# Performance work log

Hardware: AMD Instinct MI355X
Metric: run time of the kernel (lower is better)

Reference implementation:

```python
import jax, jax.numpy as jnp
import numpy as np

B, S, D, H = 4, 2048, 768, 12
DK = D // H


def setup_inputs() -> dict:
    key = jax.random.key(0)
    ks = jax.random.split(key, 13)
    s = 1.0 / np.sqrt(D)
    inp = {
        "q": jax.random.normal(ks[0], (B, S, D), jnp.float32),
        "k": jax.random.normal(ks[1], (B, S, D), jnp.float32),
        "v": jax.random.normal(ks[2], (B, S, D), jnp.float32),
        "mask": jax.random.randint(ks[3], (B, S), 0, 2, jnp.int32),
        "Wq": jax.random.normal(ks[4], (D, D), jnp.float32) * s,
        "bq": jnp.zeros((D,), jnp.float32),
        "Wk": jax.random.normal(ks[5], (D, D), jnp.float32) * s,
        "bk": jnp.zeros((D,), jnp.float32),
        "Wv": jax.random.normal(ks[6], (D, D), jnp.float32) * s,
        "bv": jnp.zeros((D,), jnp.float32),
        "Wo": jax.random.normal(ks[7], (D, D), jnp.float32) * s,
        "bo": jnp.zeros((D,), jnp.float32),
    }
    return inp


def reference(q, k, v, mask, Wq, bq, Wk, bk, Wv, bv, Wo, bo):
    b, s, d = q.shape
    # projections (torch Linear: x @ W.T + b), split into heads: [b, h, s, dk]
    Q = (q @ Wq.T + bq).reshape(b, s, H, DK).transpose(0, 2, 1, 3)
    K = (k @ Wk.T + bk).reshape(b, s, H, DK).transpose(0, 2, 1, 3)
    V = (v @ Wv.T + bv).reshape(b, s, H, DK).transpose(0, 2, 1, 3)
    scores = jnp.einsum("bhqd,bhkd->bhqk", Q, K) / jnp.sqrt(jnp.float32(DK))
    # mask [b,s] -> [b,1,s,1]: masks whole query rows (faithful to source)
    scores = jnp.where(mask[:, None, :, None] == 0, jnp.float32(-1e9), scores)
    attn = jax.nn.softmax(scores, axis=-1)  # dropout is identity at inference
    out = jnp.einsum("bhqk,bhkd->bhqd", attn, V)
    concat = out.transpose(0, 2, 1, 3).reshape(b, s, d)
    return concat @ Wo.T + bo
```

## Files before the change

### kernel.cpp

```cpp
#include <hip/hip_runtime.h>

typedef _Float16 f16;
typedef f16 f16x4 __attribute__((ext_vector_type(4)));
typedef f16 f16x8 __attribute__((ext_vector_type(8)));
typedef float f32x4 __attribute__((ext_vector_type(4)));

#define B_ 4
#define S_ 2048
#define D_ 768
#define H_ 12
#define DK_ 64

__device__ __forceinline__ void dma16(const f16* g, f16* l) {
    __builtin_amdgcn_global_load_lds(
        (__attribute__((address_space(1))) void*)(uintptr_t)g,
        (__attribute__((address_space(3))) void*)l, 16, 0, 0);
}

struct Cvt7 { const float* s[7]; f16* d[7]; int n[7]; };

__global__ __launch_bounds__(256) void cvt7_kernel(Cvt7 a)
{
    const int z = blockIdx.y;
    int i = (blockIdx.x * 256 + threadIdx.x) * 8;
    if (i >= a.n[z]) return;
    const float* __restrict__ s = a.s[z];
    float4 x = *(const float4*)(s + i);
    float4 y = *(const float4*)(s + i + 4);
    f16x8 h = {(f16)x.x, (f16)x.y, (f16)x.z, (f16)x.w,
               (f16)y.x, (f16)y.y, (f16)y.z, (f16)y.w};
    *(f16x8*)(a.d[z] + i) = h;
}

struct GemmArgs { const f16* A; const f16* W; const float* bias; float scale; void* C; int mode; };
struct GemmArgs3 { GemmArgs g[3]; };

__global__ __launch_bounds__(256, 4) void gemm_k(GemmArgs3 args)
{
    const int z = blockIdx.z;
    const f16* __restrict__ A = args.g[z].A;
    const f16* __restrict__ W = args.g[z].W;
    const float* __restrict__ bias = args.g[z].bias;
    const float scale = args.g[z].scale;
    const int mode = args.g[z].mode;

    __shared__ __align__(16) f16 As[128 * 64];
    __shared__ __align__(16) f16 Bs[128 * 64];

    const int tid = threadIdx.x, lane = tid & 63, w = tid >> 6;
    const int l15 = lane & 15, lg = lane >> 4;
    const int wm = (w >> 1) * 64, wn = (w & 1) * 64;
    const int m0 = blockIdx.y * 128, n0 = blockIdx.x * 128;

    const int lrow8 = lane >> 3;
    const int lchk8 = (lane & 7) ^ lrow8;
    const f16* gA = A + (size_t)(m0 + w * 32 + lrow8) * D_ + lchk8 * 8;
    const f16* gB = W + (size_t)(n0 + w * 32 + lrow8) * D_ + lchk8 * 8;

    f32x4 acc[4][4] = {};

    for (int kt = 0; kt < D_; kt += 64) {
        __syncthreads();
#pragma unroll
        for (int c = 0; c < 4; ++c) {
            dma16(gA + (size_t)(c * 8) * D_ + kt, &As[(w * 4 + c) * 512]);
            dma16(gB + (size_t)(c * 8) * D_ + kt, &Bs[(w * 4 + c) * 512]);
        }
        __syncthreads();
#pragma unroll
        for (int kk = 0; kk < 2; ++kk) {
            const int chk = ((kk * 4 + lg) ^ (l15 & 7)) * 8;
            f16x8 af[4], bf[4];
#pragma unroll
            for (int i = 0; i < 4; ++i)
                af[i] = *(const f16x8*)&As[(wm + i * 16 + l15) * 64 + chk];
#pragma unroll
            for (int j = 0; j < 4; ++j)
                bf[j] = *(const f16x8*)&Bs[(wn + j * 16 + l15) * 64 + chk];
#pragma unroll
            for (int i = 0; i < 4; ++i)
#pragma unroll
                for (int j = 0; j < 4; ++j)
                    acc[i][j] = __builtin_amdgcn_mfma_f32_16x16x32_f16(
                        af[i], bf[j], acc[i][j], 0, 0, 0);
        }
    }

    if (mode == 1) {
#pragma unroll
        for (int j = 0; j < 4; ++j) {
            int col = n0 + wn + j * 16 + l15;
            float bb = bias[col];
#pragma unroll
            for (int i = 0; i < 4; ++i) {
                int row = m0 + wm + i * 16 + lg * 4;
                int bI = row >> 11, sl = row & (S_ - 1);
                f16x4 o = {(f16)(acc[i][j][0] + bb), (f16)(acc[i][j][1] + bb),
                           (f16)(acc[i][j][2] + bb), (f16)(acc[i][j][3] + bb)};
                *(f16x4*)&((f16*)args.g[z].C)[((size_t)bI * D_ + col) * S_ + sl] = o;
            }
        }
    } else if (mode == 0) {
#pragma unroll
        for (int j = 0; j < 4; ++j) {
            int col = n0 + wn + j * 16 + l15;
            float bb = bias[col];
#pragma unroll
            for (int i = 0; i < 4; ++i) {
                int row = m0 + wm + i * 16 + lg * 4;
#pragma unroll
                for (int r = 0; r < 4; ++r)
                    ((f16*)args.g[z].C)[(size_t)(row + r) * D_ + col] =
                        (f16)((acc[i][j][r] + bb) * scale);
            }
        }
    } else {
#pragma unroll
        for (int j = 0; j < 4; ++j) {
            int col = n0 + wn + j * 16 + l15;
            float bb = bias[col];
#pragma unroll
            for (int i = 0; i < 4; ++i) {
                int row = m0 + wm + i * 16 + lg * 4;
#pragma unroll
                for (int r = 0; r < 4; ++r)
                    ((float*)args.g[z].C)[(size_t)(row + r) * D_ + col] =
                        acc[i][j][r] + bb;
            }
        }
    }
}

__global__ __launch_bounds__(256, 3) void attn_k(
    const f16* __restrict__ Qh, const f16* __restrict__ Kh,
    const f16* __restrict__ VhT, const int* __restrict__ mask,
    f16* __restrict__ O)
{
    __shared__ __align__(16) f16 Ks[128 * 64];
    __shared__ __align__(16) f16 Vt[64 * 128];
    const int tid = threadIdx.x, lane = tid & 63, w = tid >> 6;
    const int l15 = lane & 15, lg = lane >> 4;

    const int bid = blockIdx.x;
    const int g8 = bid & 7, j5 = bid >> 3;
    const int head_lin = g8 * 6 + (j5 >> 4);
    const int qt = j5 & 15;
    const int b = head_lin / H_, h = head_lin % H_;
    const int q0 = qt * 128;
    const int rowbase = b * S_;
    const int col0 = h * DK_;

    const int lrow8 = lane >> 3;
    const int lchk8 = (lane & 7) ^ lrow8;

    {
        const f16* Qbase = Qh + (size_t)(rowbase + q0 + w * 32 + lrow8) * D_ + col0 + lchk8 * 8;
#pragma unroll
        for (int c = 0; c < 4; ++c)
            dma16(Qbase + (size_t)(c * 8) * D_, &Ks[(w * 4 + c) * 512]);
    }
    __syncthreads();
    f16x8 qf[2][2];
#pragma unroll
    for (int ns = 0; ns < 2; ++ns) {
        float mf = (mask[rowbase + q0 + w * 32 + ns * 16 + l15] != 0) ? 1.0f : 0.0f;
#pragma unroll
        for (int kk = 0; kk < 2; ++kk) {
            f16x8 t = *(const f16x8*)&Ks[(w * 32 + ns * 16 + l15) * 64 +
                                         (((kk * 4 + lg) ^ (l15 & 7)) * 8)];
#pragma unroll
            for (int e = 0; e < 8; ++e) t[e] = (f16)((float)t[e] * mf);
            qf[ns][kk] = t;
        }
    }

    const f16* Kbase = Kh + (size_t)rowbase * D_ + col0;
    const f16* Vbase = VhT + ((size_t)b * D_ + col0) * S_;
    const int vrow4 = lane >> 4;
    const int vchk = lane & 15;

    float lrun[2] = {0.f, 0.f};
    f32x4 acc[4][2] = {};

    for (int t = 0; t < S_ / 128; ++t) {
        const int k0 = t * 128;
        __syncthreads();
#pragma unroll
        for (int c = 0; c < 4; ++c)
            dma16(Kbase + (size_t)(k0 + w * 32 + c * 8 + lrow8) * D_ + lchk8 * 8,
                  &Ks[(w * 4 + c) * 512]);
#pragma unroll
        for (int c = 0; c < 4; ++c) {
            int o = w * 4 + c;
            int drow = o * 4 + vrow4;
            int gchk = vchk ^ (drow & 15);
            dma16(Vbase + (size_t)drow * S_ + k0 + gchk * 8, &Vt[o * 512]);
        }
        __syncthreads();

        f32x4 sf[8][2] = {};
#pragma unroll
        for (int kk = 0; kk < 2; ++kk) {
            const int chk = ((kk * 4 + lg) ^ (l15 & 7)) * 8;
#pragma unroll
            for (int ms = 0; ms < 8; ++ms) {
                f16x8 kf = *(const f16x8*)&Ks[(ms * 16 + l15) * 64 + chk];
                sf[ms][0] = __builtin_amdgcn_mfma_f32_16x16x32_f16(
                    kf, qf[0][kk], sf[ms][0], 0, 0, 0);
                sf[ms][1] = __builtin_amdgcn_mfma_f32_16x16x32_f16(
                    kf, qf[1][kk], sf[ms][1], 0, 0, 0);
            }
        }

        f16x4 pf[8][2];
#pragma unroll
        for (int ns = 0; ns < 2; ++ns) {
            float rs = 0.f;
#pragma unroll
            for (int ms = 0; ms < 8; ++ms) {
                float p0 = __builtin_exp2f(sf[ms][ns][0]);
                float p1 = __builtin_exp2f(sf[ms][ns][1]);
                float p2 = __builtin_exp2f(sf[ms][ns][2]);
                float p3 = __builtin_exp2f(sf[ms][ns][3]);
                rs += (p0 + p1) + (p2 + p3);
                pf[ms][ns] = {(f16)p0, (f16)p1, (f16)p2, (f16)p3};
            }
            rs += __shfl_xor(rs, 16, 64);
            rs += __shfl_xor(rs, 32, 64);
            lrun[ns] += rs;
        }

#pragma unroll
        for (int c = 0; c < 8; ++c) {
            const int pchk = (((c * 2 + (lg >> 1)) ^ l15) * 8) + (lg & 1) * 4;
#pragma unroll
            for (int i = 0; i < 4; ++i) {
                f16x4 vf = *(const f16x4*)&Vt[(i * 16 + l15) * 128 + pchk];
                acc[i][0] = __builtin_amdgcn_mfma_f32_16x16x16f16(
                    vf, pf[c][0], acc[i][0], 0, 0, 0);
                acc[i][1] = __builtin_amdgcn_mfma_f32_16x16x16f16(
                    vf, pf[c][1], acc[i][1], 0, 0, 0);
            }
        }
    }

#pragma unroll
    for (int ns = 0; ns < 2; ++ns) {
        float inv = 1.0f / lrun[ns];
        size_t qrow = (size_t)(rowbase + q0 + w * 32 + ns * 16 + l15);
#pragma unroll
        for (int i = 0; i < 4; ++i) {
            f32x4 o = acc[i][ns] * inv;
            f16x4 ho = {(f16)o[0], (f16)o[1], (f16)o[2], (f16)o[3]};
            *(f16x4*)&O[qrow * D_ + col0 + i * 16 + lg * 4] = ho;
        }
    }
}

extern "C" void kernel_launch(void* const* d_in, const int* in_sizes, int n_in,
                              void* d_out, int out_size, void* d_ws, size_t ws_size,
                              hipStream_t stream)
{
    const float* q    = (const float*)d_in[0];
    const float* k    = (const float*)d_in[1];
    const float* v    = (const float*)d_in[2];
    const int*   mask = (const int*)d_in[3];
    const float* Wq   = (const float*)d_in[4];
    const float* bq   = (const float*)d_in[5];
    const float* Wk   = (const float*)d_in[6];
    const float* bk   = (const float*)d_in[7];
    const float* Wv   = (const float*)d_in[8];
    const float* bv   = (const float*)d_in[9];
    const float* Wo   = (const float*)d_in[10];
    const float* bo   = (const float*)d_in[11];

    const size_t nQKV = (size_t)B_ * S_ * D_;
    const size_t nW   = (size_t)D_ * D_;

    f16* qh  = (f16*)d_ws;
    f16* kh  = qh + nQKV;
    f16* vh  = kh + nQKV;
    f16* Wqh = vh + nQKV;
    f16* Wkh = Wqh + nW;
    f16* Wvh = Wkh + nW;
    f16* Woh = Wvh + nW;
    f16* Qp  = Woh + nW;
    f16* Kp  = Qp + nQKV;
    f16* VpT = Kp + nQKV;
    f16* Cp  = VpT + nQKV;

    Cvt7 cv = {{q, k, v, Wq, Wk, Wv, Wo},
               {qh, kh, vh, Wqh, Wkh, Wvh, Woh},
               {(int)nQKV, (int)nQKV, (int)nQKV, (int)nW, (int)nW, (int)nW, (int)nW}};
    cvt7_kernel<<<dim3((int)(nQKV / 8 / 256), 7), 256, 0, stream>>>(cv);

    GemmArgs3 g1 = {{{qh, Wqh, bq, 1.44269504f / 8.0f, (void*)Qp, 0},
                     {kh, Wkh, bk, 1.0f, (void*)Kp, 0},
                     {vh, Wvh, bv, 1.0f, (void*)VpT, 1}}};
    gemm_k<<<dim3(6, 64, 3), 256, 0, stream>>>(g1);

    attn_k<<<dim3(768), 256, 0, stream>>>(Qp, Kp, VpT, mask, Cp);

    GemmArgs3 g2 = {{{Cp, Woh, bo, 1.0f, d_out, 2},
                     {Cp, Woh, bo, 1.0f, d_out, 2},
                     {Cp, Woh, bo, 1.0f, d_out, 2}}};
    gemm_k<<<dim3(6, 64, 1), 256, 0, stream>>>(g2);
}
```

Before: 296.6 us.

## Double-buffer GEMM and attention LDS tiles and compute softmax row sums via MFMA

The projection GEMM now uses two K=32 LDS buffers and prefetches the next tile while computing on the current one, with a new 4-chunk swizzle. The attention kernel double-buffers its K/V tiles so the next tile's DMA overlaps the current QK^T, exp and PV work, and occupancy is lowered to 2 blocks per CU. Row sums come from an extra MFMA against a ones vector, replacing per-lane adds and cross-lane shuffles. The aim is to hide global load latency and cut VALU and shuffle work, at the cost of doubled LDS and lower occupancy.

```diff
diff --git a/kernel.cpp b/kernel.cpp
--- a/kernel.cpp
+++ b/kernel.cpp
@@ -44,46 +44,54 @@
     const float scale = args.g[z].scale;
     const int mode = args.g[z].mode;
 
-    __shared__ __align__(16) f16 As[128 * 64];
-    __shared__ __align__(16) f16 Bs[128 * 64];
+    __shared__ __align__(16) f16 As[2][128 * 32];
+    __shared__ __align__(16) f16 Bs[2][128 * 32];
 
     const int tid = threadIdx.x, lane = tid & 63, w = tid >> 6;
     const int l15 = lane & 15, lg = lane >> 4;
     const int wm = (w >> 1) * 64, wn = (w & 1) * 64;
     const int m0 = blockIdx.y * 128, n0 = blockIdx.x * 128;
 
-    const int lrow8 = lane >> 3;
-    const int lchk8 = (lane & 7) ^ lrow8;
-    const f16* gA = A + (size_t)(m0 + w * 32 + lrow8) * D_ + lchk8 * 8;
-    const f16* gB = W + (size_t)(n0 + w * 32 + lrow8) * D_ + lchk8 * 8;
+    const int r16 = lane >> 2;
+    const int rswS = (r16 & 3) ^ ((r16 >> 2) & 3);
+    const int gch = (lane & 3) ^ rswS;
+    const f16* gA = A + (size_t)(m0 + w * 32 + r16) * D_ + gch * 8;
+    const f16* gB = W + (size_t)(n0 + w * 32 + r16) * D_ + gch * 8;
+    const int rs15 = (l15 & 3) ^ ((l15 >> 2) & 3);
 
     f32x4 acc[4][4] = {};
-
-    for (int kt = 0; kt < D_; kt += 64) {
+    const int NIT = D_ / 32;
+
+#pragma unroll
+    for (int c = 0; c < 2; ++c) {
+        dma16(gA + (size_t)(c * 16) * D_, &As[0][(w * 2 + c) * 512]);
+        dma16(gB + (size_t)(c * 16) * D_, &Bs[0][(w * 2 + c) * 512]);
+    }
+
+    for (int t = 0; t < NIT; ++t) {
         __syncthreads();
-#pragma unroll
-        for (int c = 0; c < 4; ++c) {
-            dma16(gA + (size_t)(c * 8) * D_ + kt, &As[(w * 4 + c) * 512]);
-            dma16(gB + (size_t)(c * 8) * D_ + kt, &Bs[(w * 4 + c) * 512]);
-        }
-        __syncthreads();
-#pragma unroll
-        for (int kk = 0; kk < 2; ++kk) {
-            const int chk = ((kk * 4 + lg) ^ (l15 & 7)) * 8;
-            f16x8 af[4], bf[4];
-#pragma unroll
-            for (int i = 0; i < 4; ++i)
-                af[i] = *(const f16x8*)&As[(wm + i * 16 + l15) * 64 + chk];
+        if (t + 1 < NIT) {
+            const int kt = (t + 1) * 32, nb = (t + 1) & 1;
+#pragma unroll
+            for (int c = 0; c < 2; ++c) {
+                dma16(gA + (size_t)(c * 16) * D_ + kt, &As[nb][(w * 2 + c) * 512]);
+                dma16(gB + (size_t)(c * 16) * D_ + kt, &Bs[nb][(w * 2 + c) * 512]);
+            }
+        }
+        const int cb = t & 1;
+        f16x8 af[4], bf[4];
+#pragma unroll
+        for (int i = 0; i < 4; ++i)
+            af[i] = *(const f16x8*)&As[cb][(wm + i * 16 + l15) * 32 + ((lg ^ rs15) * 8)];
+#pragma unroll
+        for (int j = 0; j < 4; ++j)
+            bf[j] = *(const f16x8*)&Bs[cb][(wn + j * 16 + l15) * 32 + ((lg ^ rs15) * 8)];
+#pragma unroll
+        for (int i = 0; i < 4; ++i)
 #pragma unroll
             for (int j = 0; j < 4; ++j)
-                bf[j] = *(const f16x8*)&Bs[(wn + j * 16 + l15) * 64 + chk];
-#pragma unroll
-            for (int i = 0; i < 4; ++i)
-#pragma unroll
-                for (int j = 0; j < 4; ++j)
-                    acc[i][j] = __builtin_amdgcn_mfma_f32_16x16x32_f16(
-                        af[i], bf[j], acc[i][j], 0, 0, 0);
-        }
+                acc[i][j] = __builtin_amdgcn_mfma_f32_16x16x32_f16(
+                    af[i], bf[j], acc[i][j], 0, 0, 0);
     }
 
     if (mode == 1) {
@@ -131,13 +139,13 @@
     }
 }
 
-__global__ __launch_bounds__(256, 3) void attn_k(
+__global__ __launch_bounds__(256, 2) void attn_k(
     const f16* __restrict__ Qh, const f16* __restrict__ Kh,
     const f16* __restrict__ VhT, const int* __restrict__ mask,
     f16* __restrict__ O)
 {
-    __shared__ __align__(16) f16 Ks[128 * 64];
-    __shared__ __align__(16) f16 Vt[64 * 128];
+    __shared__ __align__(16) f16 Ks[2][128 * 64];
+    __shared__ __align__(16) f16 Vt[2][64 * 128];
     const int tid = threadIdx.x, lane = tid & 63, w = tid >> 6;
     const int l15 = lane & 15, lg = lane >> 4;
 
@@ -153,50 +161,65 @@
     const int lrow8 = lane >> 3;
     const int lchk8 = (lane & 7) ^ lrow8;
 
-    {
-        const f16* Qbase = Qh + (size_t)(rowbase + q0 + w * 32 + lrow8) * D_ + col0 + lchk8 * 8;
-#pragma unroll
-        for (int c = 0; c < 4; ++c)
-            dma16(Qbase + (size_t)(c * 8) * D_, &Ks[(w * 4 + c) * 512]);
-    }
-    __syncthreads();
-    f16x8 qf[2][2];
-#pragma unroll
-    for (int ns = 0; ns < 2; ++ns) {
-        float mf = (mask[rowbase + q0 + w * 32 + ns * 16 + l15] != 0) ? 1.0f : 0.0f;
-#pragma unroll
-        for (int kk = 0; kk < 2; ++kk) {
-            f16x8 t = *(const f16x8*)&Ks[(w * 32 + ns * 16 + l15) * 64 +
-                                         (((kk * 4 + lg) ^ (l15 & 7)) * 8)];
-#pragma unroll
-            for (int e = 0; e < 8; ++e) t[e] = (f16)((float)t[e] * mf);
-            qf[ns][kk] = t;
-        }
-    }
-
     const f16* Kbase = Kh + (size_t)rowbase * D_ + col0;
     const f16* Vbase = VhT + ((size_t)b * D_ + col0) * S_;
     const int vrow4 = lane >> 4;
     const int vchk = lane & 15;
 
-    float lrun[2] = {0.f, 0.f};
-    f32x4 acc[4][2] = {};
-
-    for (int t = 0; t < S_ / 128; ++t) {
-        const int k0 = t * 128;
-        __syncthreads();
+    {
+        const f16* Qb = Qh + (size_t)(rowbase + q0 + w * 32 + lrow8) * D_ + col0 + lchk8 * 8;
 #pragma unroll
         for (int c = 0; c < 4; ++c)
-            dma16(Kbase + (size_t)(k0 + w * 32 + c * 8 + lrow8) * D_ + lchk8 * 8,
-                  &Ks[(w * 4 + c) * 512]);
+            dma16(Qb + (size_t)(c * 8) * D_, &Ks[1][(w * 4 + c) * 512]);
+#pragma unroll
+        for (int c = 0; c < 4; ++c)
+            dma16(Kbase + (size_t)(w * 32 + c * 8 + lrow8) * D_ + lchk8 * 8,
+                  &Ks[0][(w * 4 + c) * 512]);
 #pragma unroll
         for (int c = 0; c < 4; ++c) {
             int o = w * 4 + c;
             int drow = o * 4 + vrow4;
-            int gchk = vchk ^ (drow & 15);
-            dma16(Vbase + (size_t)drow * S_ + k0 + gchk * 8, &Vt[o * 512]);
-        }
-        __syncthreads();
+            dma16(Vbase + (size_t)drow * S_ + (vchk ^ (drow & 15)) * 8,
+                  &Vt[0][o * 512]);
+        }
+    }
+    __syncthreads();
+
+    f16x8 qf[2][2];
+#pragma unroll
+    for (int ns = 0; ns < 2; ++ns) {
+        float mf = (mask[rowbase + q0 + w * 32 + ns * 16 + l15] != 0) ? 1.0f : 0.0f;
+#pragma unroll
+        for (int kk = 0; kk < 2; ++kk) {
+            f16x8 t = *(const f16x8*)&Ks[1][(w * 32 + ns * 16 + l15) * 64 +
+                                           (((kk * 4 + lg) ^ (l15 & 7)) * 8)];
+#pragma unroll
+            for (int e = 0; e < 8; ++e) t[e] = (f16)((float)t[e] * mf);
+            qf[ns][kk] = t;
+        }
+    }
+    __syncthreads();
+
+    const f16x4 kones = {(f16)1.f, (f16)1.f, (f16)1.f, (f16)1.f};
+    f32x4 acc[4][2] = {};
+    f32x4 acc_l[2] = {};
+
+    for (int t = 0; t < S_ / 128; ++t) {
+        if (t + 1 < S_ / 128) {
+            const int k0 = (t + 1) * 128, nb = (t + 1) & 1;
+#pragma unroll
+            for (int c = 0; c < 4; ++c)
+                dma16(Kbase + (size_t)(k0 + w * 32 + c * 8 + lrow8) * D_ + lchk8 * 8,
+                      &Ks[nb][(w * 4 + c) * 512]);
+#pragma unroll
+            for (int c = 0; c < 4; ++c) {
+                int o = w * 4 + c;
+                int drow = o * 4 + vrow4;
+                dma16(Vbase + (size_t)drow * S_ + k0 + (vchk ^ (drow & 15)) * 8,
+                      &Vt[nb][o * 512]);
+            }
+        }
+        const int cb = t & 1;
 
         f32x4 sf[8][2] = {};
 #pragma unroll
@@ -204,7 +227,7 @@
             const int chk = ((kk * 4 + lg) ^ (l15 & 7)) * 8;
 #pragma unroll
             for (int ms = 0; ms < 8; ++ms) {
-                f16x8 kf = *(const f16x8*)&Ks[(ms * 16 + l15) * 64 + chk];
+                f16x8 kf = *(const f16x8*)&Ks[cb][(ms * 16 + l15) * 64 + chk];
                 sf[ms][0] = __builtin_amdgcn_mfma_f32_16x16x32_f16(
                     kf, qf[0][kk], sf[ms][0], 0, 0, 0);
                 sf[ms][1] = __builtin_amdgcn_mfma_f32_16x16x32_f16(
@@ -214,39 +237,39 @@
 
         f16x4 pf[8][2];
 #pragma unroll
-        for (int ns = 0; ns < 2; ++ns) {
-            float rs = 0.f;
+        for (int ns = 0; ns < 2; ++ns)
 #pragma unroll
             for (int ms = 0; ms < 8; ++ms) {
                 float p0 = __builtin_exp2f(sf[ms][ns][0]);
                 float p1 = __builtin_exp2f(sf[ms][ns][1]);
                 float p2 = __builtin_exp2f(sf[ms][ns][2]);
                 float p3 = __builtin_exp2f(sf[ms][ns][3]);
-                rs += (p0 + p1) + (p2 + p3);
                 pf[ms][ns] = {(f16)p0, (f16)p1, (f16)p2, (f16)p3};
             }
-            rs += __shfl_xor(rs, 16, 64);
-            rs += __shfl_xor(rs, 32, 64);
-            lrun[ns] += rs;
-        }
 
 #pragma unroll
         for (int c = 0; c < 8; ++c) {
             const int pchk = (((c * 2 + (lg >> 1)) ^ l15) * 8) + (lg & 1) * 4;
 #pragma unroll
             for (int i = 0; i < 4; ++i) {
-                f16x4 vf = *(const f16x4*)&Vt[(i * 16 + l15) * 128 + pchk];
+                f16x4 vf = *(const f16x4*)&Vt[cb][(i * 16 + l15) * 128 + pchk];
                 acc[i][0] = __builtin_amdgcn_mfma_f32_16x16x16f16(
                     vf, pf[c][0], acc[i][0], 0, 0, 0);
                 acc[i][1] = __builtin_amdgcn_mfma_f32_16x16x16f16(
                     vf, pf[c][1], acc[i][1], 0, 0, 0);
             }
-        }
+            acc_l[0] = __builtin_amdgcn_mfma_f32_16x16x16f16(
+                kones, pf[c][0], acc_l[0], 0, 0, 0);
+            acc_l[1] = __builtin_amdgcn_mfma_f32_16x16x16f16(
+                kones, pf[c][1], acc_l[1], 0, 0, 0);
+        }
+
+        __syncthreads();
     }
 
 #pragma unroll
     for (int ns = 0; ns < 2; ++ns) {
-        float inv = 1.0f / lrun[ns];
+        float inv = 1.0f / acc_l[ns][0];
         size_t qrow = (size_t)(rowbase + q0 + w * 32 + ns * 16 + l15);
 #pragma unroll
         for (int i = 0; i < 4; ++i) {
```

New measurement: 318.5 us. 1.07x slower.

## Split attention key range across two blocks and combine partial results

Applied to the files above, without the earlier changes.

Splits each query tile's key loop into two halves handled by separate blocks (1536 blocks instead of 768). Each block writes unnormalized fp16 partial outputs and row sums, and a new combine kernel adds the halves and normalizes. Row sums are now computed with an extra MFMA against a ones vector instead of shuffles. Occupancy hint is raised to 4 and LDS addressing is precomputed. The split adds an extra kernel launch and extra global traffic for the partials, and the unnormalized partials are rounded to fp16, which could cost accuracy. Because there is no running max, correctness relies on Q being pre-scaled as before.

```diff
diff --git a/kernel.cpp b/kernel.cpp
--- a/kernel.cpp
+++ b/kernel.cpp
@@ -131,10 +131,11 @@
     }
 }
 
-__global__ __launch_bounds__(256, 3) void attn_k(
+__global__ __launch_bounds__(256, 4) void attn_k(
     const f16* __restrict__ Qh, const f16* __restrict__ Kh,
     const f16* __restrict__ VhT, const int* __restrict__ mask,
-    f16* __restrict__ O)
+    f16* __restrict__ Np0, f16* __restrict__ Np1,
+    float* __restrict__ Lp0, float* __restrict__ Lp1)
 {
     __shared__ __align__(16) f16 Ks[128 * 64];
     __shared__ __align__(16) f16 Vt[64 * 128];
@@ -142,9 +143,10 @@
     const int l15 = lane & 15, lg = lane >> 4;
 
     const int bid = blockIdx.x;
-    const int g8 = bid & 7, j5 = bid >> 3;
-    const int head_lin = g8 * 6 + (j5 >> 4);
-    const int qt = j5 & 15;
+    const int g8 = bid & 7, j = bid >> 3;
+    const int head_lin = g8 * 6 + (j >> 5);
+    const int qt = j & 15;
+    const int sh = (j >> 4) & 1;
     const int b = head_lin / H_, h = head_lin % H_;
     const int q0 = qt * 128;
     const int rowbase = b * S_;
@@ -153,11 +155,16 @@
     const int lrow8 = lane >> 3;
     const int lchk8 = (lane & 7) ^ lrow8;
 
+    const f16* Kbase = Kh + (size_t)(rowbase + sh * 1024) * D_ + col0;
+    const f16* Vbase = VhT + ((size_t)b * D_ + col0) * S_ + sh * 1024;
+    const int vrow4 = lane >> 4;
+    const int vchk = lane & 15;
+
     {
-        const f16* Qbase = Qh + (size_t)(rowbase + q0 + w * 32 + lrow8) * D_ + col0 + lchk8 * 8;
+        const f16* Qb = Qh + (size_t)(rowbase + q0 + w * 32 + lrow8) * D_ + col0 + lchk8 * 8;
 #pragma unroll
         for (int c = 0; c < 4; ++c)
-            dma16(Qbase + (size_t)(c * 8) * D_, &Ks[(w * 4 + c) * 512]);
+            dma16(Qb + (size_t)(c * 8) * D_, &Ks[(w * 4 + c) * 512]);
     }
     __syncthreads();
     f16x8 qf[2][2];
@@ -174,15 +181,20 @@
         }
     }
 
-    const f16* Kbase = Kh + (size_t)rowbase * D_ + col0;
-    const f16* Vbase = VhT + ((size_t)b * D_ + col0) * S_;
-    const int vrow4 = lane >> 4;
-    const int vchk = lane & 15;
-
-    float lrun[2] = {0.f, 0.f};
+    const f16* kb[2];
+#pragma unroll
+    for (int kk = 0; kk < 2; ++kk)
+        kb[kk] = &Ks[l15 * 64 + (((kk * 4 + lg) ^ (l15 & 7)) * 8)];
+    const f16* vb[8];
+#pragma unroll
+    for (int c = 0; c < 8; ++c)
+        vb[c] = &Vt[l15 * 128 + ((((c * 2 + (lg >> 1)) ^ l15) * 8) + (lg & 1) * 4)];
+
+    const f16x4 kones = {(f16)1.f, (f16)1.f, (f16)1.f, (f16)1.f};
     f32x4 acc[4][2] = {};
-
-    for (int t = 0; t < S_ / 128; ++t) {
+    f32x4 acc_l[2] = {};
+
+    for (int t = 0; t < 8; ++t) {
         const int k0 = t * 128;
         __syncthreads();
 #pragma unroll
@@ -193,68 +205,88 @@
         for (int c = 0; c < 4; ++c) {
             int o = w * 4 + c;
             int drow = o * 4 + vrow4;
-            int gchk = vchk ^ (drow & 15);
-            dma16(Vbase + (size_t)drow * S_ + k0 + gchk * 8, &Vt[o * 512]);
+            dma16(Vbase + (size_t)drow * S_ + k0 + (vchk ^ (drow & 15)) * 8,
+                  &Vt[o * 512]);
         }
         __syncthreads();
 
         f32x4 sf[8][2] = {};
 #pragma unroll
-        for (int kk = 0; kk < 2; ++kk) {
-            const int chk = ((kk * 4 + lg) ^ (l15 & 7)) * 8;
+        for (int kk = 0; kk < 2; ++kk)
 #pragma unroll
             for (int ms = 0; ms < 8; ++ms) {
-                f16x8 kf = *(const f16x8*)&Ks[(ms * 16 + l15) * 64 + chk];
+                f16x8 kf = *(const f16x8*)(kb[kk] + ms * 1024);
                 sf[ms][0] = __builtin_amdgcn_mfma_f32_16x16x32_f16(
                     kf, qf[0][kk], sf[ms][0], 0, 0, 0);
                 sf[ms][1] = __builtin_amdgcn_mfma_f32_16x16x32_f16(
                     kf, qf[1][kk], sf[ms][1], 0, 0, 0);
             }
-        }
 
         f16x4 pf[8][2];
 #pragma unroll
-        for (int ns = 0; ns < 2; ++ns) {
-            float rs = 0.f;
+        for (int ns = 0; ns < 2; ++ns)
 #pragma unroll
             for (int ms = 0; ms < 8; ++ms) {
                 float p0 = __builtin_exp2f(sf[ms][ns][0]);
                 float p1 = __builtin_exp2f(sf[ms][ns][1]);
                 float p2 = __builtin_exp2f(sf[ms][ns][2]);
                 float p3 = __builtin_exp2f(sf[ms][ns][3]);
-                rs += (p0 + p1) + (p2 + p3);
                 pf[ms][ns] = {(f16)p0, (f16)p1, (f16)p2, (f16)p3};
             }
-            rs += __shfl_xor(rs, 16, 64);
-            rs += __shfl_xor(rs, 32, 64);
-            lrun[ns] += rs;
-        }
 
 #pragma unroll
         for (int c = 0; c < 8; ++c) {
-            const int pchk = (((c * 2 + (lg >> 1)) ^ l15) * 8) + (lg & 1) * 4;
 #pragma unroll
             for (int i = 0; i < 4; ++i) {
-                f16x4 vf = *(const f16x4*)&Vt[(i * 16 + l15) * 128 + pchk];
+                f16x4 vf = *(const f16x4*)(vb[c] + i * 2048);
                 acc[i][0] = __builtin_amdgcn_mfma_f32_16x16x16f16(
                     vf, pf[c][0], acc[i][0], 0, 0, 0);
                 acc[i][1] = __builtin_amdgcn_mfma_f32_16x16x16f16(
                     vf, pf[c][1], acc[i][1], 0, 0, 0);
             }
-        }
-    }
-
+            acc_l[0] = __builtin_amdgcn_mfma_f32_16x16x16f16(
+                kones, pf[c][0], acc_l[0], 0, 0, 0);
+            acc_l[1] = __builtin_amdgcn_mfma_f32_16x16x16f16(
+                kones, pf[c][1], acc_l[1], 0, 0, 0);
+        }
+    }
+
+    f16* Np = sh ? Np1 : Np0;
+    float* Lp = sh ? Lp1 : Lp0;
 #pragma unroll
     for (int ns = 0; ns < 2; ++ns) {
-        float inv = 1.0f / lrun[ns];
-        size_t qrow = (size_t)(rowbase + q0 + w * 32 + ns * 16 + l15);
+        int q = q0 + w * 32 + ns * 16 + l15;
+        size_t qrow = (size_t)(rowbase + q);
 #pragma unroll
         for (int i = 0; i < 4; ++i) {
-            f32x4 o = acc[i][ns] * inv;
-            f16x4 ho = {(f16)o[0], (f16)o[1], (f16)o[2], (f16)o[3]};
-            *(f16x4*)&O[qrow * D_ + col0 + i * 16 + lg * 4] = ho;
-        }
-    }
+            f16x4 ho = {(f16)acc[i][ns][0], (f16)acc[i][ns][1],
+                        (f16)acc[i][ns][2], (f16)acc[i][ns][3]};
+            *(f16x4*)&Np[qrow * D_ + col0 + i * 16 + lg * 4] = ho;
+        }
+        if (lg == 0)
+            Lp[((size_t)(b * H_ + h) << 11) + q] = acc_l[ns][0];
+    }
+}
+
+__global__ __launch_bounds__(256) void combine_k(
+    const f16* __restrict__ N0, const f16* __restrict__ N1,
+    const float* __restrict__ L0, const float* __restrict__ L1,
+    f16* __restrict__ C)
+{
+    int base = (blockIdx.x * 256 + threadIdx.x) * 8;
+    int r = base / D_;
+    int c = base - r * D_;
+    int h = c >> 6;
+    int b = r >> 11, s = r & (S_ - 1);
+    int li = ((b * H_ + h) << 11) + s;
+    float inv = 1.0f / (L0[li] + L1[li]);
+    f16x8 a = *(const f16x8*)(N0 + base);
+    f16x8 d = *(const f16x8*)(N1 + base);
+    f16x8 o;
+#pragma unroll
+    for (int e = 0; e < 8; ++e)
+        o[e] = (f16)(((float)a[e] + (float)d[e]) * inv);
+    *(f16x8*)(C + base) = o;
 }
 
 extern "C" void kernel_launch(void* const* d_in, const int* in_sizes, int n_in,
@@ -276,18 +308,23 @@
 
     const size_t nQKV = (size_t)B_ * S_ * D_;
     const size_t nW   = (size_t)D_ * D_;
-
-    f16* qh  = (f16*)d_ws;
-    f16* kh  = qh + nQKV;
-    f16* vh  = kh + nQKV;
-    f16* Wqh = vh + nQKV;
+    const size_t nL   = (size_t)B_ * H_ * S_;
+
+    f16* Wqh = (f16*)d_ws;
     f16* Wkh = Wqh + nW;
     f16* Wvh = Wkh + nW;
     f16* Woh = Wvh + nW;
-    f16* Qp  = Woh + nW;
+    f16* qh  = Woh + nW;
+    f16* kh  = qh + nQKV;
+    f16* vh  = kh + nQKV;
+    f16* Qp  = vh + nQKV;
     f16* Kp  = Qp + nQKV;
     f16* VpT = Kp + nQKV;
     f16* Cp  = VpT + nQKV;
+    float* Lp0 = (float*)(Cp + nQKV);
+    float* Lp1 = Lp0 + nL;
+    f16* Np0 = qh;
+    f16* Np1 = kh;
 
     Cvt7 cv = {{q, k, v, Wq, Wk, Wv, Wo},
                {qh, kh, vh, Wqh, Wkh, Wvh, Woh},
@@ -299,7 +336,9 @@
                      {vh, Wvh, bv, 1.0f, (void*)VpT, 1}}};
     gemm_k<<<dim3(6, 64, 3), 256, 0, stream>>>(g1);
 
-    attn_k<<<dim3(768), 256, 0, stream>>>(Qp, Kp, VpT, mask, Cp);
+    attn_k<<<dim3(1536), 256, 0, stream>>>(Qp, Kp, VpT, mask, Np0, Np1, Lp0, Lp1);
+
+    combine_k<<<dim3((int)(nQKV / 8 / 256)), 256, 0, stream>>>(Np0, Np1, Lp0, Lp1, Cp);
 
     GemmArgs3 g2 = {{{Cp, Woh, bo, 1.0f, d_out, 2},
                      {Cp, Woh, bo, 1.0f, d_out, 2},
```

Measured after the change: 377.3 us. +27.2%, slower.
